# Kernel optimization log

Hardware: AMD Instinct MI355X
Metric: run time of the kernel (lower is better)

## Reference

```python
import jax, jax.numpy as jnp
import numpy as np

VOCAB = 517015      # from nn.Embedding(517015, 300)
EMB_DIM = 300       # word_emb_dim
TOTAL_WORDS = 500_000
NUM_SENTS = 25_000  # avg 20 words per sentence


def setup_inputs() -> dict:
    key = jax.random.key(0)
    k_emb, k_ids = jax.random.split(key)
    word_emb = jax.random.normal(k_emb, (VOCAB, EMB_DIM), dtype=jnp.float32) * 0.1
    word_ids = jax.random.randint(k_ids, (TOTAL_WORDS,), 0, VOCAB, dtype=jnp.int32)
    # sorted segment ids, every segment nonempty (len(sent) >= 1 in real data)
    words_per_sent = TOTAL_WORDS // NUM_SENTS
    segment_ids = jnp.arange(TOTAL_WORDS, dtype=jnp.int32) // words_per_sent
    return {
        "word_emb": word_emb,
        "word_ids": word_ids,
        "segment_ids": segment_ids,
        "num_segments": NUM_SENTS,
    }


def reference(word_emb, word_ids, segment_ids, num_segments):
    # Packed equivalent of the nested Python loops:
    # per-word embedding gather, then per-sentence mean pooling
    # (np.sum(sent, axis=0) / len(sent) in the original).
    emb = word_emb[word_ids]                                      # [T, D]
    sums = jax.ops.segment_sum(emb, segment_ids,
                               num_segments=num_segments)         # [S, D]
    counts = jax.ops.segment_sum(
        jnp.ones((word_ids.shape[0], 1), dtype=emb.dtype),
        segment_ids, num_segments=num_segments)                   # [S, 1]
    return sums / counts                                          # [S, D]
```

## Files before the change

### kernel.cpp

```cpp
#include <hip/hip_runtime.h>

#define EMB_DIM   300
#define ROW_F4    75
#define TAIL_F4   (ROW_F4 - 64)
#define ROW_BYTES (EMB_DIM * 4)

__global__ __launch_bounds__(256) void seg_starts_kernel(
        const int* __restrict__ seg, int T, int S, int* __restrict__ starts) {
    int t = blockIdx.x * 256 + threadIdx.x;
    if (t >= T) return;
    if (t == 0) {
        starts[0] = 0;
        starts[S] = T;
    } else if (seg[t] != seg[t - 1]) {
        starts[seg[t]] = t;
    }
}

template <int NR>
__device__ __forceinline__ void gather_batch(
        const char* __restrict__ embb, int my_id, int j,
        int lane, unsigned tailOff,
        float4& acc, float4& accT) {
    const char* r[NR];
    #pragma unroll
    for (int k = 0; k < NR; ++k) {
        const int id = __shfl(my_id, j + k);
        r[k] = embb + (unsigned)id * (unsigned)ROW_BYTES;
    }
    float4 m[NR], t[NR];
    #pragma unroll
    for (int k = 0; k < NR; ++k) {
        m[k] = ((const float4*)r[k])[lane];
        t[k] = *(const float4*)(r[k] + tailOff);
    }
    #pragma unroll
    for (int k = 0; k < NR; ++k) {
        acc.x  += m[k].x; acc.y  += m[k].y; acc.z  += m[k].z; acc.w  += m[k].w;
        accT.x += t[k].x; accT.y += t[k].y; accT.z += t[k].z; accT.w += t[k].w;
    }
}

__global__ __launch_bounds__(256) void emb_seg_mean_v2_kernel(
        const float* __restrict__ emb,
        const int*   __restrict__ word_ids,
        const int*   __restrict__ starts,
        float*       __restrict__ out,
        int num_segments) {
    const int lane = threadIdx.x & 63;
    const int s    = blockIdx.x * 4 + (threadIdx.x >> 6);
    if (s >= num_segments) return;

    const int start = starts[s];
    const int end   = starts[s + 1];
    const int count = end - start;

    int my_id = 0;
    if (start + lane < end) my_id = word_ids[start + lane];

    const bool tl = lane < TAIL_F4;
    const unsigned tailChunk = 64u + (unsigned)(tl ? lane : (TAIL_F4 - 1));
    const unsigned tailOff   = tailChunk * 16u;

    const char* embb = (const char*)emb;
    float4 acc  = make_float4(0.f, 0.f, 0.f, 0.f);
    float4 accT = make_float4(0.f, 0.f, 0.f, 0.f);

    const int nb = count < 64 ? count : 64;
    int j = 0;
    for (; j + 10 <= nb; j += 10)
        gather_batch<10>(embb, my_id, j, lane, tailOff, acc, accT);
    for (; j + 4 <= nb; j += 4)
        gather_batch<4>(embb, my_id, j, lane, tailOff, acc, accT);
    for (; j < nb; ++j)
        gather_batch<1>(embb, my_id, j, lane, tailOff, acc, accT);

    for (int w = start + 64; w < end; ++w) {
        const int id = word_ids[w];
        const char* r = embb + (unsigned)id * (unsigned)ROW_BYTES;
        float4 a = ((const float4*)r)[lane];
        float4 t = *(const float4*)(r + tailOff);
        acc.x  += a.x; acc.y  += a.y; acc.z  += a.z; acc.w  += a.w;
        accT.x += t.x; accT.y += t.y; accT.z += t.z; accT.w += t.w;
    }

    const float inv = 1.0f / (float)count;
    float4* __restrict__ orow = (float4*)(out + (size_t)s * EMB_DIM);
    orow[lane] = make_float4(acc.x * inv, acc.y * inv, acc.z * inv, acc.w * inv);
    if (tl)
        orow[64 + lane] = make_float4(accT.x * inv, accT.y * inv,
                                      accT.z * inv, accT.w * inv);
}

extern "C" void kernel_launch(void* const* d_in, const int* in_sizes, int n_in,
                              void* d_out, int out_size, void* d_ws, size_t ws_size,
                              hipStream_t stream) {
    const float* emb      = (const float*)d_in[0];
    const int*   word_ids = (const int*)d_in[1];
    const int*   seg_ids  = (const int*)d_in[2];
    float* out = (float*)d_out;
    int* starts = (int*)d_ws;

    const int T = in_sizes[1];
    const int S = out_size / EMB_DIM;

    seg_starts_kernel<<<(T + 255) / 256, 256, 0, stream>>>(seg_ids, T, S, starts);

    const int blocks = (S + 3) / 4;
    emb_seg_mean_v2_kernel<<<blocks, 256, 0, stream>>>(emb, word_ids, starts, out, S);
}
```

Before: 769.4 us.

## Bucket-sort words by embedding row and scatter-add into segments with atomics

Replaces the per-segment gather kernel with a pipeline that buckets word positions by the high bits of their vocabulary id (histogram, scan, atomic-rank scatter). It then processes words in id-sorted order, atomically adding each embedding row into its segment's output, and divides by counts in a final pass. The goal is locality in the random embedding reads so rows come from nearby memory. The cost is many more kernel launches, a single-block scan, zeroing the output, and per-element float atomics on output rows, which also makes results order-dependent.

```diff
diff --git a/kernel.cpp b/kernel.cpp
--- a/kernel.cpp
+++ b/kernel.cpp
@@ -3,7 +3,19 @@
 #define EMB_DIM   300
 #define ROW_F4    75
 #define TAIL_F4   (ROW_F4 - 64)
-#define ROW_BYTES (EMB_DIM * 4)
+#define ROW_BYTES 1200
+#define MAX_NB    8192
+
+
+__global__ __launch_bounds__(256) void zero_i32_kernel(int* __restrict__ p, int n) {
+    int i = blockIdx.x * 256 + threadIdx.x;
+    if (i < n) p[i] = 0;
+}
+
+__global__ __launch_bounds__(256) void zero_f4_kernel(float4* __restrict__ p, int n4) {
+    int i = blockIdx.x * 256 + threadIdx.x;
+    if (i < n4) p[i] = make_float4(0.f, 0.f, 0.f, 0.f);
+}
 
 __global__ __launch_bounds__(256) void seg_starts_kernel(
         const int* __restrict__ seg, int T, int S, int* __restrict__ starts) {
@@ -17,79 +29,134 @@
     }
 }
 
-template <int NR>
-__device__ __forceinline__ void gather_batch(
-        const char* __restrict__ embb, int my_id, int j,
-        int lane, unsigned tailOff,
-        float4& acc, float4& accT) {
-    const char* r[NR];
+__global__ __launch_bounds__(256) void hist_kernel(
+        const int* __restrict__ ids, int T, int shift, int* __restrict__ hist) {
+    int t = blockIdx.x * 256 + threadIdx.x;
+    if (t < T) atomicAdd(&hist[((unsigned)ids[t]) >> shift], 1);
+}
+
+__global__ __launch_bounds__(1024) void scan_kernel(
+        const int* __restrict__ hist, int* __restrict__ cursor, int NB) {
+    __shared__ int part[1024];
+    const int tid = threadIdx.x;
+    int c[8];
+    int sum = 0;
+    const int base_i = tid * 8;
     #pragma unroll
-    for (int k = 0; k < NR; ++k) {
-        const int id = __shfl(my_id, j + k);
-        r[k] = embb + (unsigned)id * (unsigned)ROW_BYTES;
+    for (int k = 0; k < 8; ++k) {
+        int i = base_i + k;
+        c[k] = (i < NB) ? hist[i] : 0;
+        sum += c[k];
     }
-    float4 m[NR], t[NR];
+    part[tid] = sum;
+    __syncthreads();
+    for (int off = 1; off < 1024; off <<= 1) {
+        int add = (tid >= off) ? part[tid - off] : 0;
+        __syncthreads();
+        part[tid] += add;
+        __syncthreads();
+    }
+    int run = part[tid] - sum;
     #pragma unroll
-    for (int k = 0; k < NR; ++k) {
-        m[k] = ((const float4*)r[k])[lane];
-        t[k] = *(const float4*)(r[k] + tailOff);
-    }
-    #pragma unroll
-    for (int k = 0; k < NR; ++k) {
-        acc.x  += m[k].x; acc.y  += m[k].y; acc.z  += m[k].z; acc.w  += m[k].w;
-        accT.x += t[k].x; accT.y += t[k].y; accT.z += t[k].z; accT.w += t[k].w;
+    for (int k = 0; k < 8; ++k) {
+        int i = base_i + k;
+        if (i < NB) cursor[i] = run;
+        run += c[k];
     }
 }
 
-__global__ __launch_bounds__(256) void emb_seg_mean_v2_kernel(
+__global__ __launch_bounds__(256) void scatter_rank_kernel(
+        const int* __restrict__ ids, int T, int shift,
+        int* __restrict__ cursor, int* __restrict__ sw) {
+    int t = blockIdx.x * 256 + threadIdx.x;
+    if (t >= T) return;
+    int b = ((unsigned)ids[t]) >> shift;
+    int r = atomicAdd(&cursor[b], 1);
+    sw[r] = t;
+}
+
+__global__ __launch_bounds__(256) void scatter_add_kernel(
         const float* __restrict__ emb,
-        const int*   __restrict__ word_ids,
-        const int*   __restrict__ starts,
+        const int*   __restrict__ ids,
+        const int*   __restrict__ seg,
+        const int*   __restrict__ sw,
         float*       __restrict__ out,
-        int num_segments) {
+        int T) {
+    const int lane = threadIdx.x & 63;
+    const int wid  = threadIdx.x >> 6;
+    const int base_rank = (blockIdx.x * 4 + wid) * 4;
+    if (base_rank >= T) return;
+
+    const bool tl = lane < TAIL_F4;
+    const unsigned mainOff = (unsigned)lane * 16u;
+    const unsigned tailOff = 1024u + (unsigned)(tl ? lane : (TAIL_F4 - 1)) * 16u;
+    const char* embb = (const char*)emb;
+
+    if (base_rank + 4 <= T) {
+        int tk[4], sg[4];
+        const char* r[4];
+        #pragma unroll
+        for (int k = 0; k < 4; ++k) tk[k] = sw[base_rank + k];
+        #pragma unroll
+        for (int k = 0; k < 4; ++k) {
+            sg[k] = seg[tk[k]];
+            r[k]  = embb + (unsigned)ids[tk[k]] * (unsigned)ROW_BYTES;
+        }
+        float4 m[4], tt[4];
+        #pragma unroll
+        for (int k = 0; k < 4; ++k) {
+            m[k]  = *(const float4*)(r[k] + mainOff);
+            tt[k] = *(const float4*)(r[k] + tailOff);
+        }
+        #pragma unroll
+        for (int k = 0; k < 4; ++k) {
+            float* __restrict__ orow = out + (size_t)sg[k] * EMB_DIM;
+            atomicAdd(orow + lane * 4 + 0, m[k].x);
+            atomicAdd(orow + lane * 4 + 1, m[k].y);
+            atomicAdd(orow + lane * 4 + 2, m[k].z);
+            atomicAdd(orow + lane * 4 + 3, m[k].w);
+            if (tl) {
+                atomicAdd(orow + 256 + lane * 4 + 0, tt[k].x);
+                atomicAdd(orow + 256 + lane * 4 + 1, tt[k].y);
+                atomicAdd(orow + 256 + lane * 4 + 2, tt[k].z);
+                atomicAdd(orow + 256 + lane * 4 + 3, tt[k].w);
+            }
+        }
+    } else {
+        for (int k = 0; k < T - base_rank; ++k) {
+            int t  = sw[base_rank + k];
+            int sgk = seg[t];
+            const char* r = embb + (unsigned)ids[t] * (unsigned)ROW_BYTES;
+            float4 m  = *(const float4*)(r + mainOff);
+            float4 tt = *(const float4*)(r + tailOff);
+            float* __restrict__ orow = out + (size_t)sgk * EMB_DIM;
+            atomicAdd(orow + lane * 4 + 0, m.x);
+            atomicAdd(orow + lane * 4 + 1, m.y);
+            atomicAdd(orow + lane * 4 + 2, m.z);
+            atomicAdd(orow + lane * 4 + 3, m.w);
+            if (tl) {
+                atomicAdd(orow + 256 + lane * 4 + 0, tt.x);
+                atomicAdd(orow + 256 + lane * 4 + 1, tt.y);
+                atomicAdd(orow + 256 + lane * 4 + 2, tt.z);
+                atomicAdd(orow + 256 + lane * 4 + 3, tt.w);
+            }
+        }
+    }
+}
+
+__global__ __launch_bounds__(256) void mean_kernel(
+        const int* __restrict__ starts, float* __restrict__ out, int S) {
     const int lane = threadIdx.x & 63;
     const int s    = blockIdx.x * 4 + (threadIdx.x >> 6);
-    if (s >= num_segments) return;
-
-    const int start = starts[s];
-    const int end   = starts[s + 1];
-    const int count = end - start;
-
-    int my_id = 0;
-    if (start + lane < end) my_id = word_ids[start + lane];
-
-    const bool tl = lane < TAIL_F4;
-    const unsigned tailChunk = 64u + (unsigned)(tl ? lane : (TAIL_F4 - 1));
-    const unsigned tailOff   = tailChunk * 16u;
-
-    const char* embb = (const char*)emb;
-    float4 acc  = make_float4(0.f, 0.f, 0.f, 0.f);
-    float4 accT = make_float4(0.f, 0.f, 0.f, 0.f);
-
-    const int nb = count < 64 ? count : 64;
-    int j = 0;
-    for (; j + 10 <= nb; j += 10)
-        gather_batch<10>(embb, my_id, j, lane, tailOff, acc, accT);
-    for (; j + 4 <= nb; j += 4)
-        gather_batch<4>(embb, my_id, j, lane, tailOff, acc, accT);
-    for (; j < nb; ++j)
-        gather_batch<1>(embb, my_id, j, lane, tailOff, acc, accT);
-
-    for (int w = start + 64; w < end; ++w) {
-        const int id = word_ids[w];
-        const char* r = embb + (unsigned)id * (unsigned)ROW_BYTES;
-        float4 a = ((const float4*)r)[lane];
-        float4 t = *(const float4*)(r + tailOff);
-        acc.x  += a.x; acc.y  += a.y; acc.z  += a.z; acc.w  += a.w;
-        accT.x += t.x; accT.y += t.y; accT.z += t.z; accT.w += t.w;
+    if (s >= S) return;
+    const float inv = 1.0f / (float)(starts[s + 1] - starts[s]);
+    float4* __restrict__ orow = (float4*)(out + (size_t)s * EMB_DIM);
+    float4 a = orow[lane];
+    orow[lane] = make_float4(a.x * inv, a.y * inv, a.z * inv, a.w * inv);
+    if (lane < TAIL_F4) {
+        float4 b = orow[64 + lane];
+        orow[64 + lane] = make_float4(b.x * inv, b.y * inv, b.z * inv, b.w * inv);
     }
-
-    const float inv = 1.0f / (float)count;
-    float4* __restrict__ orow = (float4*)(out + (size_t)s * EMB_DIM);
-    orow[lane] = make_float4(acc.x * inv, acc.y * inv, acc.z * inv, acc.w * inv);
-    if (tl)
-        orow[64 + lane] = make_float4(accT.x * inv, accT.y * inv,
-                                      accT.z * inv, accT.w * inv);
 }
 
 extern "C" void kernel_launch(void* const* d_in, const int* in_sizes, int n_in,
@@ -99,13 +166,33 @@
     const int*   word_ids = (const int*)d_in[1];
     const int*   seg_ids  = (const int*)d_in[2];
     float* out = (float*)d_out;
-    int* starts = (int*)d_ws;
 
     const int T = in_sizes[1];
     const int S = out_size / EMB_DIM;
+    const int vocab = in_sizes[0] / EMB_DIM;
 
+    int* W = (int*)d_ws;
+    int* starts = W;
+    int* hist   = W + 32768;
+    int* cursor = W + 32768 + MAX_NB;
+    int* sw     = W + 32768 + 2 * MAX_NB;
+
+    int shift = 7;
+    while ((((unsigned)(vocab - 1)) >> shift) + 1 > MAX_NB) ++shift;
+    const int NB = (((unsigned)(vocab - 1)) >> shift) + 1;
+
+    zero_i32_kernel<<<(NB + 255) / 256, 256, 0, stream>>>(hist, NB);
+    zero_f4_kernel<<<(S * ROW_F4 + 255) / 256, 256, 0, stream>>>(
+        (float4*)out, S * ROW_F4);
     seg_starts_kernel<<<(T + 255) / 256, 256, 0, stream>>>(seg_ids, T, S, starts);
+    hist_kernel<<<(T + 255) / 256, 256, 0, stream>>>(word_ids, T, shift, hist);
+    scan_kernel<<<1, 1024, 0, stream>>>(hist, cursor, NB);
+    scatter_rank_kernel<<<(T + 255) / 256, 256, 0, stream>>>(
+        word_ids, T, shift, cursor, sw);
 
-    const int blocks = (S + 3) / 4;
-    emb_seg_mean_v2_kernel<<<blocks, 256, 0, stream>>>(emb, word_ids, starts, out, S);
+    const int nwaves = (T + 3) / 4;
+    scatter_add_kernel<<<(nwaves + 3) / 4, 256, 0, stream>>>(
+        emb, word_ids, seg_ids, sw, out, T);
+
+    mean_kernel<<<(S + 3) / 4, 256, 0, stream>>>(starts, out, S);
 }
```

Measured after the change: 2.838 ms. 3.69x slower.
